# Kernel tuning notes

Measured on AMD Instinct MI355X. Metric: run time of the kernel, lower is better.

## Reference

```python
import jax, jax.numpy as jnp
import numpy as np

NHEAD = 8
LN_EPS = 1e-5   # torch nn.LayerNorm default
ATT_EPS = 1e-6  # LinearAttention eps


def layernorm(x, g, b):
    mu = jnp.mean(x, axis=-1, keepdims=True)
    var = jnp.mean((x - mu) ** 2, axis=-1, keepdims=True)
    return (x - mu) / jnp.sqrt(var + LN_EPS) * g + b


def setup_inputs() -> dict:
    key = jax.random.key(0)
    ks = jax.random.split(key, 9)
    B, C, H, W = 8, 256, 64, 64
    d = C
    w = lambda k, shp: (jax.random.normal(k, shp, dtype=jnp.float32) * 0.02)
    return {
        "x": jax.random.normal(ks[0], (B, C, H, W), dtype=jnp.float32),
        "source": jax.random.normal(ks[1], (B, C, H, W), dtype=jnp.float32),
        # weights stored [in, out] (already transposed vs torch's [out, in])
        "Wq": w(ks[2], (d, d)),
        "Wk": w(ks[3], (d, d)),
        "Wv": w(ks[4], (d, d)),
        "Wm": w(ks[5], (d, d)),
        "W1": w(ks[6], (2 * d, 2 * d)),
        "W2": w(ks[7], (2 * d, d)),
        "g1": jnp.ones((d,), jnp.float32),
        "b1": jnp.zeros((d,), jnp.float32),
        "g2": jnp.ones((d,), jnp.float32),
        "b2": jnp.zeros((d,), jnp.float32),
    }


def reference(x, source, Wq, Wk, Wv, Wm, W1, W2, g1, b1, g2, b2):
    B, C, H, W = x.shape
    L = H * W
    dim = C // NHEAD
    xs = x.reshape(B, C, L).transpose(0, 2, 1)        # [B, L, C]
    ss = source.reshape(B, C, L).transpose(0, 2, 1)   # [B, L, C]

    q = (xs @ Wq).reshape(B, L, NHEAD, dim)
    k = (ss @ Wk).reshape(B, L, NHEAD, dim)
    v = (ss @ Wv).reshape(B, L, NHEAD, dim)

    # linear attention with elu+1 feature map
    Q = jax.nn.elu(q) + 1.0
    K = jax.nn.elu(k) + 1.0
    vals = v / L
    KV = jnp.einsum('nshd,nshv->nhdv', K, vals)                    # [B, h, d, d]
    Z = 1.0 / (jnp.einsum('nlhd,nhd->nlh', Q, K.sum(axis=1)) + ATT_EPS)
    msg = jnp.einsum('nlhd,nhdv,nlh->nlhv', Q, KV, Z) * L          # [B, L, h, d]

    msg = msg.reshape(B, L, C) @ Wm
    msg = layernorm(msg, g1, b1)
    msg = jax.nn.relu(jnp.concatenate([xs, msg], axis=-1) @ W1) @ W2
    msg = layernorm(msg, g2, b2)

    out = xs + msg
    return out.transpose(0, 2, 1).reshape(B, C, H, W)
```

## Files before the change

### kernel.cpp

```cpp
#include <hip/hip_runtime.h>

typedef unsigned short u16;
typedef __bf16 bf16x8 __attribute__((ext_vector_type(8)));
typedef float f32x4 __attribute__((ext_vector_type(4)));

__device__ __forceinline__ u16 f2bf(float f) {
  unsigned int u = __float_as_uint(f);
  u += 0x7fffu + ((u >> 16) & 1u);
  return (u16)(u >> 16);
}
__device__ __forceinline__ float bf2f(u16 v) {
  return __uint_as_float(((unsigned)v) << 16);
}

#define GLDS16(gp, lp)                                                   \
  __builtin_amdgcn_global_load_lds(                                      \
      (const __attribute__((address_space(1))) unsigned int*)(gp),       \
      (__attribute__((address_space(3))) unsigned int*)(lp), 16, 0, 0)

#define OFF_WQ     0u
#define OFF_WK     131072u
#define OFF_WV     262144u
#define OFF_WM     393216u
#define OFF_W1     524288u
#define OFF_W2     1048576u
#define OFF_CAT    1310720u
#define OFF_SSB    34865152u
#define OFF_KVPROJ 68419584u
#define OFF_KS     152567808u
#define OFF_KVP    152576000u
#define OFF_KSP    154673152u
#define OFF_WC     154740736u

__global__ __launch_bounds__(256) void prep_kernel(
    const float* __restrict__ x, const float* __restrict__ srcp,
    u16* __restrict__ cat, u16* __restrict__ ssb,
    const float* __restrict__ Wq, const float* __restrict__ Wk,
    const float* __restrict__ Wv, const float* __restrict__ Wm,
    const float* __restrict__ W1, const float* __restrict__ W2,
    u16* __restrict__ dq, u16* __restrict__ dk, u16* __restrict__ dv,
    u16* __restrict__ dm, u16* __restrict__ d1, u16* __restrict__ d2) {
  __shared__ float s[64 * 65];
  const int bid = blockIdx.x;
  const int t = threadIdx.x;
  if (bid < 4096) {
    const int bx = bid & 63, by = (bid >> 6) & 3, z = bid >> 8;
    const float* src = z < 8 ? x : srcp;
    u16* dst = z < 8 ? cat : ssb;
    const int dstride = z < 8 ? 512 : 256;
    const int b = z & 7;
    const int lt = bx * 64, ct = by * 64;
    const int cl = t >> 2, loff = (t & 3) * 16;
#pragma unroll
    for (int j = 0; j < 4; ++j) {
      float4 v = *reinterpret_cast<const float4*>(
          src + ((size_t)b * 256 + ct + cl) * 4096 + lt + loff + j * 4);
      s[cl * 65 + loff + j * 4 + 0] = v.x;
      s[cl * 65 + loff + j * 4 + 1] = v.y;
      s[cl * 65 + loff + j * 4 + 2] = v.z;
      s[cl * 65 + loff + j * 4 + 3] = v.w;
    }
    __syncthreads();
#pragma unroll
    for (int i = 0; i < 2; ++i) {
      int id = t + i * 256;
      int ll = id >> 3, cg = id & 7;
      unsigned pk[4];
#pragma unroll
      for (int j = 0; j < 4; ++j) {
        unsigned lo = f2bf(s[(cg * 8 + j * 2) * 65 + ll]);
        unsigned hi = f2bf(s[(cg * 8 + j * 2 + 1) * 65 + ll]);
        pk[j] = lo | (hi << 16);
      }
      uint4 val = {pk[0], pk[1], pk[2], pk[3]};
      *reinterpret_cast<uint4*>(
          dst + ((size_t)b * 4096 + lt + ll) * dstride + ct + cg * 8) = val;
    }
  } else {
    const int wb = bid - 4096;
    const float* src; u16* dst; int Kd, Nd, tt;
    if (wb < 64)       { src = Wq; dst = dq; Kd = 256; Nd = 256; tt = wb; }
    else if (wb < 128) { src = Wk; dst = dk; Kd = 256; Nd = 256; tt = wb - 64; }
    else if (wb < 192) { src = Wv; dst = dv; Kd = 256; Nd = 256; tt = wb - 128; }
    else if (wb < 256) { src = Wm; dst = dm; Kd = 256; Nd = 256; tt = wb - 192; }
    else if (wb < 512) { src = W1; dst = d1; Kd = 512; Nd = 512; tt = wb - 256; }
    else               { src = W2; dst = d2; Kd = 512; Nd = 256; tt = wb - 512; }
    int ntn = Nd >> 5;
    int kt = (tt / ntn) * 32, nt = (tt % ntn) * 32;
    int tx = t & 31, ty = t >> 5;
#pragma unroll
    for (int i = 0; i < 4; ++i)
      s[(ty + i * 8) * 33 + tx] = src[(size_t)(kt + ty + i * 8) * Nd + nt + tx];
    __syncthreads();
#pragma unroll
    for (int i = 0; i < 4; ++i)
      dst[(size_t)(nt + ty + i * 8) * Kd + kt + tx] = f2bf(s[tx * 33 + ty + i * 8]);
  }
}

template <int EPI>
__global__ __launch_bounds__(512) void gemm256_kernel(
    const u16* __restrict__ A, int lda, const u16* __restrict__ Wt, int K,
    u16* __restrict__ outp, int ldo) {
  __shared__ alignas(16) u16 sA[128 * 64];
  __shared__ alignas(16) u16 sB[256 * 64];
  const int t = threadIdx.x;
  int bid = blockIdx.x;
  int xcd = bid & 7, i0 = bid >> 3;
  const int m0 = (xcd * 32 + (i0 >> 1)) * 128;
  const int n0 = (i0 & 1) * 256;
  const int w = t >> 6, lane = t & 63;
  const int wm = (w >> 2) * 64, wn = (w & 3) * 64;
  const int lr = lane & 15, lk = lane >> 4;
  f32x4 acc[4][4] = {};
  const int nkt = K >> 6;
  for (int kt = 0; kt < nkt; ++kt) {
    __syncthreads();
#pragma unroll
    for (int i = 0; i < 2; ++i) {
      int id = t + i * 512, row = id >> 3, ch = (id & 7) << 3;
      GLDS16(A + (size_t)(m0 + row) * lda + kt * 64 + ch, sA + id * 8);
    }
#pragma unroll
    for (int i = 0; i < 4; ++i) {
      int id = t + i * 512, row = id >> 3, ch = (id & 7) << 3;
      GLDS16(Wt + (size_t)(n0 + row) * K + kt * 64 + ch, sB + id * 8);
    }
    __syncthreads();
    bf16x8 af[4][2], bfr[4][2];
#pragma unroll
    for (int f = 0; f < 4; ++f) {
#pragma unroll
      for (int ks = 0; ks < 2; ++ks) {
        af[f][ks] = *reinterpret_cast<const bf16x8*>(
            &sA[(wm + f * 16 + lr) * 64 + ks * 32 + lk * 8]);
        bfr[f][ks] = *reinterpret_cast<const bf16x8*>(
            &sB[(wn + f * 16 + lr) * 64 + ks * 32 + lk * 8]);
      }
    }
#pragma unroll
    for (int ks = 0; ks < 2; ++ks)
#pragma unroll
      for (int fm = 0; fm < 4; ++fm)
#pragma unroll
        for (int fn = 0; fn < 4; ++fn)
          acc[fm][fn] = __builtin_amdgcn_mfma_f32_16x16x32_bf16(
              af[fm][ks], bfr[fn][ks], acc[fm][fn], 0, 0, 0);
  }
  const int r0 = (lane >> 4) * 4, c0 = lane & 15;
#pragma unroll
  for (int fm = 0; fm < 4; ++fm) {
#pragma unroll
    for (int fn = 0; fn < 4; ++fn) {
      int gr = m0 + wm + fm * 16 + r0;
      int gc = n0 + wn + fn * 16 + c0;
#pragma unroll
      for (int r = 0; r < 4; ++r) {
        float v = acc[fm][fn][r];
        if (EPI == 3) v = v > 0.f ? v : 0.f;
        if (EPI == 4) v = (gc < 256) ? (v > 0.f ? v + 1.f : __expf(v)) : v * (1.f / 4096.f);
        outp[(size_t)(gr + r) * ldo + gc] = f2bf(v);
      }
    }
  }
}

__global__ __launch_bounds__(256) void kv_partial_kernel(
    const u16* __restrict__ KVproj, float* __restrict__ KVp,
    float* __restrict__ KSp) {
  __shared__ alignas(16) float sK[64][32];
  __shared__ alignas(16) float sV[64][32];
  const int bh = blockIdx.x, sl = blockIdx.y;
  const int b = bh >> 3, h = bh & 7;
  const int t = threadIdx.x;
  const int lrow = t >> 2, lcol = (t & 3) * 8;
  const int d = t >> 3, vg = (t & 7) * 4;
  float a0 = 0, a1 = 0, a2 = 0, a3 = 0, ks = 0;
  for (int lt = 0; lt < 512; lt += 64) {
    __syncthreads();
    size_t roff = ((size_t)b * 4096 + sl * 512 + lt + lrow) * 512 + h * 32 + lcol;
    uint4 kq = *reinterpret_cast<const uint4*>(KVproj + roff);
    uint4 vq = *reinterpret_cast<const uint4*>(KVproj + roff + 256);
    float* dk = &sK[lrow][lcol];
    float* dv = &sV[lrow][lcol];
#pragma unroll
    for (int j = 0; j < 4; ++j) {
      unsigned uk = ((const unsigned*)&kq)[j];
      unsigned uv = ((const unsigned*)&vq)[j];
      dk[2 * j] = __uint_as_float(uk << 16);
      dk[2 * j + 1] = __uint_as_float(uk & 0xffff0000u);
      dv[2 * j] = __uint_as_float(uv << 16);
      dv[2 * j + 1] = __uint_as_float(uv & 0xffff0000u);
    }
    __syncthreads();
#pragma unroll 8
    for (int i = 0; i < 64; ++i) {
      float kd = sK[i][d];
      a0 += kd * sV[i][vg + 0];
      a1 += kd * sV[i][vg + 1];
      a2 += kd * sV[i][vg + 2];
      a3 += kd * sV[i][vg + 3];
      ks += kd;
    }
  }
  float* o = KVp + (size_t)sl * 65536 + bh * 1024 + d * 32 + vg;
  o[0] = a0; o[1] = a1; o[2] = a2; o[3] = a3;
  if ((t & 7) == 0) KSp[(size_t)sl * 2048 + bh * 32 + d] = ks;
}

__global__ __launch_bounds__(256) void kvred_wcomb_kernel(
    const float* __restrict__ KVp, const float* __restrict__ KSp,
    const u16* __restrict__ wmt, u16* __restrict__ wc,
    float* __restrict__ Ksum) {
  __shared__ float sKV[8 * 1032];
  const int b = blockIdx.x >> 3, nc = blockIdx.x & 7;
  const int t = threadIdx.x;
#pragma unroll
  for (int i = 0; i < 32; ++i) {
    int idx = t + i * 256;
    float s = 0.f;
#pragma unroll
    for (int sl = 0; sl < 8; ++sl) s += KVp[(size_t)sl * 65536 + b * 8192 + idx];
    sKV[(idx >> 10) * 1032 + (idx & 1023)] = s;
  }
  if (nc == 0) {
    float s = 0.f;
#pragma unroll
    for (int sl = 0; sl < 8; ++sl) s += KSp[(size_t)sl * 2048 + b * 256 + t];
    Ksum[b * 256 + t] = s;
  }
  __syncthreads();
  const int n = nc * 32 + (t >> 3), h = t & 7;
  float wmv[32];
  const u16* wmrow = wmt + (size_t)n * 256 + h * 32;
#pragma unroll
  for (int v = 0; v < 32; ++v) wmv[v] = bf2f(wmrow[v]);
  unsigned pk[16];
  const float* kvh = &sKV[h * 1032];
#pragma unroll
  for (int dp = 0; dp < 16; ++dp) {
    unsigned lohi[2];
#pragma unroll
    for (int e = 0; e < 2; ++e) {
      int d = dp * 2 + e;
      const float* kv = kvh + d * 32;
      float s = 0.f;
#pragma unroll
      for (int v = 0; v < 32; ++v) s += kv[v] * wmv[v];
      lohi[e] = f2bf(s);
    }
    pk[dp] = lohi[0] | (lohi[1] << 16);
  }
  uint4* dst = (uint4*)(wc + ((size_t)b * 256 + n) * 256 + h * 32);
#pragma unroll
  for (int j = 0; j < 4; ++j) {
    uint4 val = {pk[j * 4], pk[j * 4 + 1], pk[j * 4 + 2], pk[j * 4 + 3]};
    dst[j] = val;
  }
}

__global__ __launch_bounds__(512) void qmsg_kernel(
    const u16* __restrict__ cat, const u16* __restrict__ WqT,
    const float* __restrict__ KSb, const u16* __restrict__ wc,
    const float* __restrict__ g1, const float* __restrict__ b1,
    u16* __restrict__ catout) {
  __shared__ alignas(16) char smem[57344];
  u16* sA = (u16*)smem;
  u16* sB = (u16*)(smem + 16384);
  u16* Qlds = (u16*)smem;
  u16* sWc = (u16*)(smem + 35840);
  float* scr = (float*)(smem + 52224);
  const int t = threadIdx.x;
  const int m0 = blockIdx.x * 128;
  const int b = m0 >> 12;
  const int w = t >> 6, lane = t & 63;
  const int wm = (w >> 2) * 64, wn = (w & 3) * 64;
  const int lr = lane & 15, lk = lane >> 4;
  f32x4 acc[4][4] = {};
  float ksv[4];
#pragma unroll
  for (int fn = 0; fn < 4; ++fn) ksv[fn] = KSb[b * 256 + wn + fn * 16 + lr];
  for (int kt = 0; kt < 4; ++kt) {
    __syncthreads();
#pragma unroll
    for (int i = 0; i < 2; ++i) {
      int id = t + i * 512, row = id >> 3, ch = (id & 7) << 3;
      GLDS16(cat + (size_t)(m0 + row) * 512 + kt * 64 + ch, sA + id * 8);
    }
#pragma unroll
    for (int i = 0; i < 4; ++i) {
      int id = t + i * 512, row = id >> 3, ch = (id & 7) << 3;
      GLDS16(WqT + (size_t)row * 256 + kt * 64 + ch, sB + id * 8);
    }
    __syncthreads();
    bf16x8 af[4][2], bfr[4][2];
#pragma unroll
    for (int f = 0; f < 4; ++f)
#pragma unroll
      for (int ks = 0; ks < 2; ++ks) {
        af[f][ks] = *(const bf16x8*)&sA[(wm + f * 16 + lr) * 64 + ks * 32 + lk * 8];
        bfr[f][ks] = *(const bf16x8*)&sB[(wn + f * 16 + lr) * 64 + ks * 32 + lk * 8];
      }
#pragma unroll
    for (int ks = 0; ks < 2; ++ks)
#pragma unroll
      for (int fm = 0; fm < 4; ++fm)
#pragma unroll
        for (int fn = 0; fn < 4; ++fn)
          acc[fm][fn] = __builtin_amdgcn_mfma_f32_16x16x32_bf16(
              af[fm][ks], bfr[fn][ks], acc[fm][fn], 0, 0, 0);
  }
#pragma unroll
  for (int fm = 0; fm < 4; ++fm)
#pragma unroll
    for (int r = 0; r < 4; ++r) {
      float q[4];
#pragma unroll
      for (int fn = 0; fn < 4; ++fn) {
        float v = acc[fm][fn][r];
        q[fn] = v > 0.f ? v + 1.f : __expf(v);
      }
      float zd0 = q[0] * ksv[0] + q[1] * ksv[1];
      float zd1 = q[2] * ksv[2] + q[3] * ksv[3];
#pragma unroll
      for (int off = 1; off < 16; off <<= 1) {
        zd0 += __shfl_xor(zd0, off);
        zd1 += __shfl_xor(zd1, off);
      }
      float z0 = 4096.f / (zd0 + 1e-6f);
      float z1 = 4096.f / (zd1 + 1e-6f);
      acc[fm][0][r] = q[0] * z0; acc[fm][1][r] = q[1] * z0;
      acc[fm][2][r] = q[2] * z1; acc[fm][3][r] = q[3] * z1;
    }
  f32x4 acc2[4][4] = {};
  const u16* Bw = wc + (size_t)b * 65536;
  for (int hh = 0; hh < 2; ++hh) {
    __syncthreads();
    if ((wn >> 7) == hh) {
#pragma unroll
      for (int fm = 0; fm < 4; ++fm)
#pragma unroll
        for (int fn = 0; fn < 4; ++fn)
#pragma unroll
          for (int r = 0; r < 4; ++r)
            Qlds[(wm + fm * 16 + lk * 4 + r) * 136 + (wn & 64) + fn * 16 + lr] =
                f2bf(acc[fm][fn][r]);
    }
    __syncthreads();
    for (int kc2 = 0; kc2 < 4; ++kc2) {
#pragma unroll
      for (int i = 0; i < 2; ++i) {
        int id = t + i * 512, row = id >> 2, ch = (id & 3) << 3;
        GLDS16(Bw + (size_t)row * 256 + hh * 128 + kc2 * 32 +
                   (ch ^ ((row & 3) << 3)), sWc + id * 8);
      }
      __syncthreads();
      bf16x8 a2[4], b2f[4];
#pragma unroll
      for (int f = 0; f < 4; ++f)
        a2[f] = *(const bf16x8*)&Qlds[(wm + f * 16 + lr) * 136 + kc2 * 32 + lk * 8];
#pragma unroll
      for (int fn = 0; fn < 4; ++fn) {
        int br = wn + fn * 16 + lr;
        b2f[fn] = *(const bf16x8*)&sWc[br * 32 + ((lk * 8) ^ ((br & 3) << 3))];
      }
#pragma unroll
      for (int fm = 0; fm < 4; ++fm)
#pragma unroll
        for (int fn = 0; fn < 4; ++fn)
          acc2[fm][fn] = __builtin_amdgcn_mfma_f32_16x16x32_bf16(
              a2[fm], b2f[fn], acc2[fm][fn], 0, 0, 0);
      __syncthreads();
    }
  }
#pragma unroll
  for (int fm = 0; fm < 4; ++fm)
#pragma unroll
    for (int r = 0; r < 4; ++r) {
      float s = 0.f, sq = 0.f;
#pragma unroll
      for (int fn = 0; fn < 4; ++fn) {
        float a = acc2[fm][fn][r];
        s += a; sq += a * a;
      }
#pragma unroll
      for (int off = 1; off < 16; off <<= 1) {
        s += __shfl_xor(s, off);
        sq += __shfl_xor(sq, off);
      }
      if (lr == 0) {
        int row = wm + fm * 16 + lk * 4 + r;
        scr[row * 8 + (w & 3) * 2] = s;
        scr[row * 8 + (w & 3) * 2 + 1] = sq;
      }
    }
  __syncthreads();
  float gvs[4], bvs[4];
#pragma unroll
  for (int fn = 0; fn < 4; ++fn) {
    gvs[fn] = g1[wn + fn * 16 + lr];
    bvs[fn] = b1[wn + fn * 16 + lr];
  }
#pragma unroll
  for (int fm = 0; fm < 4; ++fm)
#pragma unroll
    for (int r = 0; r < 4; ++r) {
      int row = wm + fm * 16 + lk * 4 + r;
      float s = 0.f, sq = 0.f;
#pragma unroll
      for (int j = 0; j < 4; ++j) {
        s += scr[row * 8 + j * 2];
        sq += scr[row * 8 + j * 2 + 1];
      }
      float mu = s * (1.f / 256.f);
      float var = sq * (1.f / 256.f) - mu * mu;
      float rstd = rsqrtf(var + 1e-5f);
#pragma unroll
      for (int fn = 0; fn < 4; ++fn) {
        float y = (acc2[fm][fn][r] - mu) * rstd * gvs[fn] + bvs[fn];
        catout[(size_t)(m0 + row) * 512 + 256 + wn + fn * 16 + lr] = f2bf(y);
      }
    }
}

__global__ __launch_bounds__(512) void mlp2_tail_kernel(
    const u16* __restrict__ hidden, const u16* __restrict__ W2T,
    const float* __restrict__ g2, const float* __restrict__ b2,
    const u16* __restrict__ catp, float* __restrict__ out) {
  __shared__ alignas(16) char smem[16384 + 32768 + 4096 + 2048];
  u16* sA = (u16*)smem;
  u16* sB = (u16*)(smem + 16384);
  float* scr = (float*)(smem + 49152);
  float* sG = (float*)(smem + 53248);
  float* T = (float*)smem;
  const int t = threadIdx.x;
  const int m0 = blockIdx.x * 128;
  const int b = m0 >> 12, l0 = m0 & 4095;
  if (t < 256) { sG[t] = g2[t]; sG[256 + t] = b2[t]; }
  const int w = t >> 6, lane = t & 63;
  const int wm = (w >> 2) * 64, wn = (w & 3) * 64;
  const int lr = lane & 15, lk = lane >> 4;
  f32x4 acc[4][4] = {};
  for (int kt = 0; kt < 8; ++kt) {
    __syncthreads();
#pragma unroll
    for (int i = 0; i < 2; ++i) {
      int id = t + i * 512, row = id >> 3, chn = (id & 7) << 3;
      GLDS16(hidden + (size_t)(m0 + row) * 512 + kt * 64 + chn, sA + id * 8);
    }
#pragma unroll
    for (int i = 0; i < 4; ++i) {
      int id = t + i * 512, row = id >> 3, chn = (id & 7) << 3;
      GLDS16(W2T + (size_t)row * 512 + kt * 64 + chn, sB + id * 8);
    }
    __syncthreads();
    bf16x8 af[4][2], bfr[4][2];
#pragma unroll
    for (int f = 0; f < 4; ++f) {
#pragma unroll
      for (int ks = 0; ks < 2; ++ks) {
        af[f][ks] = *reinterpret_cast<const bf16x8*>(
            &sA[(wm + f * 16 + lr) * 64 + ks * 32 + lk * 8]);
        bfr[f][ks] = *reinterpret_cast<const bf16x8*>(
            &sB[(wn + f * 16 + lr) * 64 + ks * 32 + lk * 8]);
      }
    }
#pragma unroll
    for (int ks = 0; ks < 2; ++ks)
#pragma unroll
      for (int fm = 0; fm < 4; ++fm)
#pragma unroll
        for (int fn = 0; fn < 4; ++fn)
          acc[fm][fn] = __builtin_amdgcn_mfma_f32_16x16x32_bf16(
              af[fm][ks], bfr[fn][ks], acc[fm][fn], 0, 0, 0);
  }
#pragma unroll
  for (int fm = 0; fm < 4; ++fm)
#pragma unroll
    for (int r = 0; r < 4; ++r) {
      float s = 0.f, sq = 0.f;
#pragma unroll
      for (int fn = 0; fn < 4; ++fn) {
        float a = acc[fm][fn][r];
        s += a; sq += a * a;
      }
#pragma unroll
      for (int off = 1; off < 16; off <<= 1) {
        s += __shfl_xor(s, off);
        sq += __shfl_xor(sq, off);
      }
      if (lr == 0) {
        int row = wm + fm * 16 + lk * 4 + r;
        scr[row * 8 + (w & 3) * 2] = s;
        scr[row * 8 + (w & 3) * 2 + 1] = sq;
      }
    }
  __syncthreads();
  float gvs[4], bvs[4];
#pragma unroll
  for (int fn = 0; fn < 4; ++fn) {
    gvs[fn] = sG[wn + fn * 16 + lr];
    bvs[fn] = sG[256 + wn + fn * 16 + lr];
  }
#pragma unroll
  for (int fm = 0; fm < 4; ++fm)
#pragma unroll
    for (int r = 0; r < 4; ++r) {
      int row = wm + fm * 16 + lk * 4 + r;
      float s = 0.f, sq = 0.f;
#pragma unroll
      for (int j = 0; j < 4; ++j) {
        s += scr[row * 8 + j * 2];
        sq += scr[row * 8 + j * 2 + 1];
      }
      float mu = s * (1.f / 256.f);
      float var = sq * (1.f / 256.f) - mu * mu;
      float rstd = rsqrtf(var + 1e-5f);
#pragma unroll
      for (int fn = 0; fn < 4; ++fn) {
        float xs = bf2f(catp[(size_t)(m0 + row) * 512 + wn + fn * 16 + lr]);
        acc[fm][fn][r] = (acc[fm][fn][r] - mu) * rstd * gvs[fn] + bvs[fn] + xs;
      }
    }
  __syncthreads();
  for (int cc = 0; cc < 4; ++cc) {
    if ((w & 3) == cc) {
#pragma unroll
      for (int fm = 0; fm < 4; ++fm)
#pragma unroll
        for (int fn = 0; fn < 4; ++fn)
#pragma unroll
          for (int r = 0; r < 4; ++r)
            T[(fn * 16 + lr) * 129 + wm + fm * 16 + lk * 4 + r] = acc[fm][fn][r];
    }
    __syncthreads();
#pragma unroll
    for (int i = 0; i < 4; ++i) {
      int idx = t + i * 512;
      int cT = idx >> 5, lq = (idx & 31) * 4;
      int cg = cc * 64 + cT;
      size_t o = ((size_t)b * 256 + cg) * 4096 + l0 + lq;
      float4 ov;
      ov.x = T[cT * 129 + lq];
      ov.y = T[cT * 129 + lq + 1];
      ov.z = T[cT * 129 + lq + 2];
      ov.w = T[cT * 129 + lq + 3];
      *reinterpret_cast<float4*>(out + o) = ov;
    }
    __syncthreads();
  }
}

extern "C" void kernel_launch(void* const* d_in, const int* in_sizes, int n_in,
                              void* d_out, int out_size, void* d_ws, size_t ws_size,
                              hipStream_t stream) {
  (void)in_sizes; (void)n_in; (void)out_size; (void)ws_size;
  const float* x = (const float*)d_in[0];
  const float* srcp = (const float*)d_in[1];
  const float* Wq = (const float*)d_in[2];
  const float* Wk = (const float*)d_in[3];
  const float* Wv = (const float*)d_in[4];
  const float* Wm = (const float*)d_in[5];
  const float* W1 = (const float*)d_in[6];
  const float* W2 = (const float*)d_in[7];
  const float* g1 = (const float*)d_in[8];
  const float* b1 = (const float*)d_in[9];
  const float* g2 = (const float*)d_in[10];
  const float* b2 = (const float*)d_in[11];
  float* out = (float*)d_out;
  char* ws = (char*)d_ws;

  u16* wqt = (u16*)(ws + OFF_WQ);
  u16* wkvt = (u16*)(ws + OFF_WK);
  u16* wkt = (u16*)(ws + OFF_WK);
  u16* wvt = (u16*)(ws + OFF_WV);
  u16* wmt = (u16*)(ws + OFF_WM);
  u16* w1t = (u16*)(ws + OFF_W1);
  u16* w2t = (u16*)(ws + OFF_W2);
  u16* cat = (u16*)(ws + OFF_CAT);
  u16* ssb = (u16*)(ws + OFF_SSB);
  u16* kvproj = (u16*)(ws + OFF_KVPROJ);
  float* KSb = (float*)(ws + OFF_KS);
  float* KVp = (float*)(ws + OFF_KVP);
  float* KSp = (float*)(ws + OFF_KSP);
  u16* wcombT = (u16*)(ws + OFF_WC);
  u16* hidden = kvproj;

  dim3 blk(256);
  prep_kernel<<<dim3(4736), blk, 0, stream>>>(x, srcp, cat, ssb,
                                              Wq, Wk, Wv, Wm, W1, W2,
                                              wqt, wkt, wvt, wmt, w1t, w2t);
  gemm256_kernel<4><<<dim3(512), dim3(512), 0, stream>>>(ssb, 256, wkvt, 256, kvproj, 512);
  kv_partial_kernel<<<dim3(64, 8), blk, 0, stream>>>(kvproj, KVp, KSp);
  kvred_wcomb_kernel<<<dim3(64), blk, 0, stream>>>(KVp, KSp, wmt, wcombT, KSb);
  qmsg_kernel<<<dim3(256), dim3(512), 0, stream>>>(cat, wqt, KSb, wcombT, g1, b1, cat);
  gemm256_kernel<3><<<dim3(512), dim3(512), 0, stream>>>(cat, 512, w1t, 512, hidden, 512);
  mlp2_tail_kernel<<<dim3(256), dim3(512), 0, stream>>>(hidden, w2t, g2, b2, cat, out);
}
```

Before: 154.5 us.

## Replace MLP1 GEMM with 256x256-tile 8-phase pipelined kernel and remap KV partial grid

Replaces the generic gemm256 ReLU path for the first MLP projection with a dedicated kernel. It uses 256x256 output tiles, 128KB of double-buffered swizzled LDS filled by direct global-to-LDS loads, and an 8-phase schedule that interleaves staging with MFMA work under explicit waitcnt, barriers and setprio. Block indices are mapped so each XCD gets contiguous row tiles, aiming for better L2 reuse. kv_partial now uses a flattened 1D grid with batch as the fastest-varying index, which spreads batches across XCDs. The trade-off is one block per CU with a large register accumulator, fragile manual synchronisation, and a host attribute call on every launch.

Result: faster. 150.8 us (-2.4%).

```diff
diff --git a/kernel.cpp b/kernel.cpp
--- a/kernel.cpp
+++ b/kernel.cpp
@@ -17,6 +17,8 @@
   __builtin_amdgcn_global_load_lds(                                      \
       (const __attribute__((address_space(1))) unsigned int*)(gp),       \
       (__attribute__((address_space(3))) unsigned int*)(lp), 16, 0, 0)
+
+#define SWZ(row, colb) ((colb) ^ (((row) & 7) << 4))
 
 #define OFF_WQ     0u
 #define OFF_WK     131072u
@@ -157,12 +159,115 @@
 #pragma unroll
       for (int r = 0; r < 4; ++r) {
         float v = acc[fm][fn][r];
-        if (EPI == 3) v = v > 0.f ? v : 0.f;
         if (EPI == 4) v = (gc < 256) ? (v > 0.f ? v + 1.f : __expf(v)) : v * (1.f / 4096.f);
         outp[(size_t)(gr + r) * ldo + gc] = f2bf(v);
       }
     }
   }
+}
+
+__global__ __launch_bounds__(512, 1) void mlp1_8ph_kernel(
+    const u16* __restrict__ A, const u16* __restrict__ Bw,
+    u16* __restrict__ outp) {
+  extern __shared__ char smem[];
+  const int t = threadIdx.x;
+  int bid = blockIdx.x;
+  int xcd = bid & 7, i0 = bid >> 3;
+  const int m0 = (xcd * 16 + (i0 >> 1)) * 256;
+  const int n0 = (i0 & 1) * 256;
+  const int w = t >> 6, lane = t & 63;
+  const int wn2 = w * 32;
+  const int lr = lane & 15, lk = lane >> 4;
+  f32x4 acc[16][2] = {};
+
+#define STAGE_A(db, h, kt)                                                  \
+  {                                                                         \
+    _Pragma("unroll") for (int i_ = 0; i_ < 2; ++i_) {                      \
+      int id_ = t + i_ * 512;                                               \
+      int row_ = id_ >> 3, colb_ = (id_ & 7) * 16;                          \
+      GLDS16(A + (size_t)(m0 + (h) * 128 + row_) * 512 + (kt) * 64 +        \
+                 (SWZ(row_, colb_) >> 1),                                   \
+             smem + (db) * 32768 + (h) * 16384 + id_ * 16);                 \
+    }                                                                       \
+  }
+#define STAGE_B(db, h, kt)                                                  \
+  {                                                                         \
+    _Pragma("unroll") for (int i_ = 0; i_ < 2; ++i_) {                      \
+      int id_ = t + i_ * 512;                                               \
+      int row_ = id_ >> 3, colb_ = (id_ & 7) * 16;                          \
+      GLDS16(Bw + (size_t)(n0 + (h) * 128 + row_) * 512 + (kt) * 64 +       \
+                 (SWZ(row_, colb_) >> 1),                                   \
+             smem + 65536 + (db) * 32768 + (h) * 16384 + id_ * 16);         \
+    }                                                                       \
+  }
+
+  STAGE_A(0, 0, 0); STAGE_A(0, 1, 0); STAGE_B(0, 0, 0); STAGE_B(0, 1, 0);
+  STAGE_A(1, 0, 1);
+  asm volatile("s_waitcnt vmcnt(0)" ::: "memory");
+  __builtin_amdgcn_s_barrier();
+
+  for (int it = 0; it < 4; ++it) {
+    const int e = 2 * it, o = e + 1;
+#pragma unroll
+    for (int p = 0; p < 8; ++p) {
+      const int db = p >> 2;
+      const int ah = (p >> 1) & 1;
+      const int ks = p & 1;
+      bf16x8 af[8], bf[2];
+#pragma unroll
+      for (int j = 0; j < 8; ++j) {
+        int mf = ah * 8 + j;
+        int rowh = (mf & 7) * 16 + lr;
+        af[j] = *(const bf16x8*)(smem + db * 32768 + (mf >> 3) * 16384 +
+                                 rowh * 128 + SWZ(rowh, ks * 64 + lk * 16));
+      }
+#pragma unroll
+      for (int fn = 0; fn < 2; ++fn) {
+        int col = wn2 + fn * 16 + lr;
+        int rowh = col & 127;
+        bf[fn] = *(const bf16x8*)(smem + 65536 + db * 32768 +
+                                  (col >> 7) * 16384 + rowh * 128 +
+                                  SWZ(rowh, ks * 64 + lk * 16));
+      }
+      if (p == 0) STAGE_A(1, 1, o)
+      else if (p == 1) STAGE_B(1, 0, o)
+      else if (p == 2) { if (e + 2 < 8) STAGE_A(0, 0, e + 2) }
+      else if (p == 3) STAGE_B(1, 1, o)
+      else if (p == 4) { if (e + 2 < 8) STAGE_B(0, 0, e + 2) }
+      else if (p == 5) { if (e + 2 < 8) STAGE_B(0, 1, e + 2) }
+      else if (p == 6) { if (e + 2 < 8) STAGE_A(0, 1, e + 2) }
+      else             { if (o + 2 < 8) STAGE_A(1, 0, o + 2) }
+      __builtin_amdgcn_s_barrier();
+      asm volatile("s_waitcnt lgkmcnt(0)" ::: "memory");
+      __builtin_amdgcn_sched_barrier(0);
+      __builtin_amdgcn_s_setprio(1);
+#pragma unroll
+      for (int j = 0; j < 8; ++j)
+#pragma unroll
+        for (int fn = 0; fn < 2; ++fn)
+          acc[ah * 8 + j][fn] = __builtin_amdgcn_mfma_f32_16x16x32_bf16(
+              af[j], bf[fn], acc[ah * 8 + j][fn], 0, 0, 0);
+      __builtin_amdgcn_s_setprio(0);
+      if (p == 3) asm volatile("s_waitcnt vmcnt(0)" ::: "memory");
+      if (p == 7) asm volatile("s_waitcnt vmcnt(2)" ::: "memory");
+      __builtin_amdgcn_s_barrier();
+    }
+  }
+  const int r0 = (lane >> 4) * 4, c0 = lane & 15;
+#pragma unroll
+  for (int mf = 0; mf < 16; ++mf)
+#pragma unroll
+    for (int fn = 0; fn < 2; ++fn) {
+      int gr = m0 + mf * 16 + r0;
+      int gc = n0 + wn2 + fn * 16 + c0;
+#pragma unroll
+      for (int r = 0; r < 4; ++r) {
+        float v = acc[mf][fn][r];
+        outp[(size_t)(gr + r) * 512 + gc] = f2bf(v > 0.f ? v : 0.f);
+      }
+    }
+#undef STAGE_A
+#undef STAGE_B
 }
 
 __global__ __launch_bounds__(256) void kv_partial_kernel(
@@ -170,8 +275,8 @@
     float* __restrict__ KSp) {
   __shared__ alignas(16) float sK[64][32];
   __shared__ alignas(16) float sV[64][32];
-  const int bh = blockIdx.x, sl = blockIdx.y;
-  const int b = bh >> 3, h = bh & 7;
+  const int id = blockIdx.x;
+  const int b = id & 7, h = (id >> 3) & 7, sl = id >> 6;
   const int t = threadIdx.x;
   const int lrow = t >> 2, lcol = (t & 3) * 8;
   const int d = t >> 3, vg = (t & 7) * 4;
@@ -203,6 +308,7 @@
       ks += kd;
     }
   }
+  const int bh = b * 8 + h;
   float* o = KVp + (size_t)sl * 65536 + bh * 1024 + d * 32 + vg;
   o[0] = a0; o[1] = a1; o[2] = a2; o[3] = a3;
   if ((t & 7) == 0) KSp[(size_t)sl * 2048 + bh * 32 + d] = ks;
@@ -586,14 +692,19 @@
   u16* wcombT = (u16*)(ws + OFF_WC);
   u16* hidden = kvproj;
 
+  static bool attr_done = false;
+  hipFuncSetAttribute((const void*)mlp1_8ph_kernel,
+                      hipFuncAttributeMaxDynamicSharedMemorySize, 131072);
+  (void)attr_done;
+
   dim3 blk(256);
   prep_kernel<<<dim3(4736), blk, 0, stream>>>(x, srcp, cat, ssb,
                                               Wq, Wk, Wv, Wm, W1, W2,
                                               wqt, wkt, wvt, wmt, w1t, w2t);
   gemm256_kernel<4><<<dim3(512), dim3(512), 0, stream>>>(ssb, 256, wkvt, 256, kvproj, 512);
-  kv_partial_kernel<<<dim3(64, 8), blk, 0, stream>>>(kvproj, KVp, KSp);
+  kv_partial_kernel<<<dim3(512), blk, 0, stream>>>(kvproj, KVp, KSp);
   kvred_wcomb_kernel<<<dim3(64), blk, 0, stream>>>(KVp, KSp, wmt, wcombT, KSb);
   qmsg_kernel<<<dim3(256), dim3(512), 0, stream>>>(cat, wqt, KSb, wcombT, g1, b1, cat);
-  gemm256_kernel<3><<<dim3(512), dim3(512), 0, stream>>>(cat, 512, w1t, 512, hidden, 512);
+  mlp1_8ph_kernel<<<dim3(256), dim3(512), 131072, stream>>>(cat, w1t, hidden);
   mlp2_tail_kernel<<<dim3(256), dim3(512), 0, stream>>>(hidden, w2t, g2, b2, cat, out);
 }
```
